# Performance work log

Hardware: AMD Instinct MI355X
Metric: run time of the kernel (lower is better)

Reference implementation:

```python
import jax, jax.numpy as jnp
import numpy as np

LN_EPS = 1e-5

def _ln(x, w, b):
    mu = jnp.mean(x, axis=-1, keepdims=True)
    var = jnp.var(x, axis=-1, keepdims=True)
    return (x - mu) * jax.lax.rsqrt(var + LN_EPS) * w + b

def setup_inputs() -> dict:
    key = jax.random.key(0)
    ks = jax.random.split(key, 16)
    B, T, N = 32, 1024, 77
    D, TD, TE = 512, 256, 2048
    s = lambda fan: 1.0 / np.sqrt(fan)
    return {
        "x": jax.random.normal(ks[0], (B, T, D), jnp.float32),
        "xf": jax.random.normal(ks[1], (B, N, TD), jnp.float32),
        "emb": jax.random.normal(ks[2], (B, TE), jnp.float32),
        "src_mask": jnp.ones((B, T), jnp.float32),
        "cond_type": jax.random.randint(ks[3], (B,), 0, 100, jnp.int64),
        "norm_w": jnp.ones((D,), jnp.float32),
        "norm_b": jnp.zeros((D,), jnp.float32),
        "tnorm_w": jnp.ones((TD,), jnp.float32),
        "tnorm_b": jnp.zeros((TD,), jnp.float32),
        "Wq": jax.random.normal(ks[4], (D, D), jnp.float32) * s(D),
        "bq": jnp.zeros((D,), jnp.float32),
        "Wk": jax.random.normal(ks[5], (D, TD), jnp.float32) * s(TD),
        "bk": jnp.zeros((D,), jnp.float32),
        "Wv": jax.random.normal(ks[6], (D, TD), jnp.float32) * s(TD),
        "bv": jnp.zeros((D,), jnp.float32),
        "emb_w": jax.random.normal(ks[7], (2 * D, TE), jnp.float32) * s(TE),
        "emb_b": jnp.zeros((2 * D,), jnp.float32),
        "snorm_w": jnp.ones((D,), jnp.float32),
        "snorm_b": jnp.zeros((D,), jnp.float32),
        "Wout": jax.random.normal(ks[8], (D, D), jnp.float32) * s(D),
        "bout": jnp.zeros((D,), jnp.float32),
    }

def reference(x, xf, emb, src_mask, cond_type,
              norm_w, norm_b, tnorm_w, tnorm_b,
              Wq, bq, Wk, bk, Wv, bv,
              emb_w, emb_b, snorm_w, snorm_b, Wout, bout):
    B, T, D = x.shape
    N = xf.shape[1]
    H = 8
    dh = D // H
    # projections (no 1/sqrt(dh) scaling, per original)
    q = (_ln(x, norm_w, norm_b) @ Wq.T + bq).reshape(B, T, H, dh)
    xf_n = _ln(xf, tnorm_w, tnorm_b)
    k = (xf_n @ Wk.T + bk).reshape(B, N, H, dh)
    # cond_type gating: text_cond_type = (cond_type % 10 > 0)
    tc = (cond_type % 10 > 0).astype(x.dtype)  # [B]
    bias = (1.0 - tc)[:, None, None, None] * -1000000.0  # [B,1,1,1]
    attn = jnp.einsum('bthd,bnhd->btnh', q, k) + bias
    attn = jax.nn.softmax(attn, axis=2)  # over keys N
    v = (xf_n @ Wv.T + bv) * tc[:, None, None]
    v = v.reshape(B, N, H, dh)
    y = jnp.einsum('btnh,bnhd->bthd', attn, v).reshape(B, T, D)
    # StylizationBlock: silu->linear on emb -> scale/shift, ln, silu->linear, residual
    e = jax.nn.silu(emb) @ emb_w.T + emb_b  # [B, 2D]
    scale, shift = jnp.split(e[:, None, :], 2, axis=2)  # [B,1,D] each
    h = _ln(y, snorm_w, snorm_b) * (1.0 + scale) + shift
    h = jax.nn.silu(h) @ Wout.T + bout
    return x + h
```

## Files before the change

kernel.cpp:

```cpp
#include <hip/hip_runtime.h>
#include <math.h>

#define B_   32
#define T_   1024
#define N_   77
#define D_   512
#define TD_  256
#define TE_  2048
#define H_   8
#define DH_  64

typedef short bf16x8 __attribute__((ext_vector_type(8)));
typedef float f32x4  __attribute__((ext_vector_type(4)));

__device__ __forceinline__ float sigmoidf_fast(float x) {
    return 1.0f / (1.0f + __expf(-x));
}

__device__ __forceinline__ unsigned short f2b(float f) {
    unsigned int u = __float_as_uint(f);
    unsigned int r = u + 0x7FFFu + ((u >> 16) & 1u);
    return (unsigned short)(r >> 16);
}

__device__ __forceinline__ float b2f(short us) {
    return __uint_as_float(((unsigned int)(unsigned short)us) << 16);
}

#define GL16(g, l) __builtin_amdgcn_global_load_lds(                         \
    (const __attribute__((address_space(1))) unsigned int*)(g),              \
    (__attribute__((address_space(3))) unsigned int*)(l), 16, 0, 0)

__global__ __launch_bounds__(256) void ln_xf_kernel(
    const float* __restrict__ x, const float* __restrict__ w, const float* __restrict__ b,
    unsigned short* __restrict__ outb)
{
    int row = blockIdx.x * 4 + (threadIdx.x >> 6);
    int lane = threadIdx.x & 63;
    const float* rp = x + (size_t)row * TD_ + lane * 4;
    float4 v = *(const float4*)rp;
    float s  = v.x + v.y + v.z + v.w;
    float ss = v.x*v.x + v.y*v.y + v.z*v.z + v.w*v.w;
    #pragma unroll
    for (int off = 32; off; off >>= 1) {
        s  += __shfl_xor(s, off);
        ss += __shfl_xor(ss, off);
    }
    float m = s * (1.f / TD_);
    float r = rsqrtf(ss * (1.f / TD_) - m * m + 1e-5f);
    float4 wv = *(const float4*)(w + lane * 4);
    float4 bv = *(const float4*)(b + lane * 4);
    ushort4 o;
    o.x = f2b((v.x - m) * r * wv.x + bv.x);
    o.y = f2b((v.y - m) * r * wv.y + bv.y);
    o.z = f2b((v.z - m) * r * wv.z + bv.z);
    o.w = f2b((v.w - m) * r * wv.w + bv.w);
    *(ushort4*)(outb + (size_t)row * TD_ + lane * 4) = o;
}

__global__ __launch_bounds__(256) void conv_weights_kernel(
    const float* __restrict__ Wq, const float* __restrict__ Wout,
    const float* __restrict__ Wk, const float* __restrict__ Wv,
    unsigned short* __restrict__ wqb, unsigned short* __restrict__ wob,
    unsigned short* __restrict__ wkvb)
{
    int bid = blockIdx.x;
    const float* src; unsigned short* dst;
    if (bid < 128)      { src = Wq;   dst = wqb; }
    else if (bid < 256) { src = Wout; dst = wob;               bid -= 128; }
    else if (bid < 320) { src = Wk;   dst = wkvb;              bid -= 256; }
    else                { src = Wv;   dst = wkvb + D_ * TD_;   bid -= 320; }
    int idx = (bid * 256 + threadIdx.x) * 8;
    float4 v0 = *(const float4*)(src + idx);
    float4 v1 = *(const float4*)(src + idx + 4);
    ushort4 o0 = {f2b(v0.x), f2b(v0.y), f2b(v0.z), f2b(v0.w)};
    ushort4 o1 = {f2b(v1.x), f2b(v1.y), f2b(v1.z), f2b(v1.w)};
    *(ushort4*)(dst + idx)     = o0;
    *(ushort4*)(dst + idx + 4) = o1;
}

__global__ __launch_bounds__(256) void kv_gemm_kernel(
    const unsigned short* __restrict__ Ab,
    const unsigned short* __restrict__ Wb,
    const float* __restrict__ bkp, const float* __restrict__ bvp,
    const int*   __restrict__ cond,
    unsigned short* __restrict__ kout, unsigned short* __restrict__ vout)
{
    constexpr int K = TD_;
    __shared__ __align__(16) unsigned short As[128 * 32];
    __shared__ __align__(16) unsigned short Bs[128 * 32];

    const int tid  = threadIdx.x;
    int id = blockIdx.x;
    int swz = (id & 7) * 20 + (id >> 3);
    const int m0 = (swz >> 3) * 128;
    const int n0 = (swz & 7) * 128;
    const int lane = tid & 63;
    const int w    = tid >> 6;
    const int l15  = lane & 15;
    const int quad = lane >> 4;
    const int wm   = (w >> 1) * 64;
    const int wn   = (w & 1) * 64;

    const int row_a = tid >> 2;
    const int ck    = (tid & 3) ^ ((row_a >> 1) & 3);
    const int sc    = (quad ^ ((l15 >> 1) & 3)) << 3;

    f32x4 acc[4][4];
    #pragma unroll
    for (int i = 0; i < 4; i++)
        #pragma unroll
        for (int j = 0; j < 4; j++)
            acc[i][j] = (f32x4){0.f, 0.f, 0.f, 0.f};

    const char* gAbase = (const char*)Ab + ((size_t)(m0 + row_a) * K) * 2 + ck * 16;
    const char* gBbase = (const char*)Wb + ((size_t)(n0 + row_a) * K) * 2 + ck * 16;
    char* lA = (char*)As + tid * 16;
    char* lB = (char*)Bs + tid * 16;

    for (int k0 = 0; k0 < K; k0 += 32) {
        const char* gA = gAbase + k0 * 2;
        const char* gB = gBbase + k0 * 2;
        GL16(gA, lA);
        GL16(gA + (size_t)64 * K * 2, lA + 4096);
        GL16(gB, lB);
        GL16(gB + (size_t)64 * K * 2, lB + 4096);
        __syncthreads();

        bf16x8 af[4], bfr[4];
        #pragma unroll
        for (int i = 0; i < 4; i++)
            af[i] = *(const bf16x8*)&As[(wm + i * 16 + l15) * 32 + sc];
        #pragma unroll
        for (int j = 0; j < 4; j++)
            bfr[j] = *(const bf16x8*)&Bs[(wn + j * 16 + l15) * 32 + sc];
        #pragma unroll
        for (int i = 0; i < 4; i++)
            #pragma unroll
            for (int j = 0; j < 4; j++)
                acc[i][j] = __builtin_amdgcn_mfma_f32_16x16x32_bf16(af[i], bfr[j], acc[i][j], 0, 0, 0);
        __syncthreads();
    }

    #pragma unroll
    for (int i = 0; i < 4; i++) {
        int mbase = m0 + wm + i * 16 + quad * 4;
        #pragma unroll
        for (int j = 0; j < 4; j++) {
            int n = n0 + wn + j * 16 + l15;
            bool isv = n >= D_;
            int nn = isv ? n - D_ : n;
            float bn = isv ? bvp[nn] : bkp[nn];
            unsigned short* outp = isv ? vout : kout;
            #pragma unroll
            for (int r = 0; r < 4; r++) {
                int m = mbase + r;
                if (m >= B_ * N_) continue;
                float v = acc[i][j][r] + bn;
                if (isv) {
                    int bi = m / N_;
                    v = ((cond[bi] % 10) > 0) ? v : 0.f;
                }
                outp[(size_t)m * D_ + nn] = f2b(v);
            }
        }
    }
}

__global__ __launch_bounds__(256) void emb_gemm_kernel(
    const float* __restrict__ emb, const float* __restrict__ W,
    float* __restrict__ e)
{
    int wid = blockIdx.x * 4 + (threadIdx.x >> 6);
    int lane = threadIdx.x & 63;
    int ngrp = wid >> 3;
    int bgrp = wid & 7;

    float acc[4][4] = {};
    #pragma unroll 2
    for (int it = 0; it < 8; it++) {
        int k = (it * 64 + lane) * 4;
        float4 sv[4], wv[4];
        #pragma unroll
        for (int bi = 0; bi < 4; bi++) {
            float4 t = *(const float4*)&emb[(size_t)(bgrp * 4 + bi) * TE_ + k];
            t.x *= sigmoidf_fast(t.x);
            t.y *= sigmoidf_fast(t.y);
            t.z *= sigmoidf_fast(t.z);
            t.w *= sigmoidf_fast(t.w);
            sv[bi] = t;
        }
        #pragma unroll
        for (int ni = 0; ni < 4; ni++)
            wv[ni] = *(const float4*)&W[(size_t)(ngrp * 4 + ni) * TE_ + k];
        #pragma unroll
        for (int bi = 0; bi < 4; bi++)
            #pragma unroll
            for (int ni = 0; ni < 4; ni++) {
                acc[bi][ni] = fmaf(sv[bi].x, wv[ni].x, acc[bi][ni]);
                acc[bi][ni] = fmaf(sv[bi].y, wv[ni].y, acc[bi][ni]);
                acc[bi][ni] = fmaf(sv[bi].z, wv[ni].z, acc[bi][ni]);
                acc[bi][ni] = fmaf(sv[bi].w, wv[ni].w, acc[bi][ni]);
            }
    }
    #pragma unroll
    for (int bi = 0; bi < 4; bi++)
        #pragma unroll
        for (int ni = 0; ni < 4; ni++) {
            float a = acc[bi][ni];
            #pragma unroll
            for (int off = 32; off; off >>= 1) a += __shfl_xor(a, off);
            if (lane == 0)
                e[(size_t)(bgrp * 4 + bi) * 1024 + ngrp * 4 + ni] = a;
        }
}

__global__ __launch_bounds__(256) void prep_q_kernel(
    const float* __restrict__ x, const float* __restrict__ w, const float* __restrict__ b,
    unsigned short* __restrict__ outb)
{
    int row = blockIdx.x * 4 + (threadIdx.x >> 6);
    int lane = threadIdx.x & 63;
    const float* rp = x + (size_t)row * D_ + lane * 8;
    float4 v0 = *(const float4*)rp;
    float4 v1 = *(const float4*)(rp + 4);
    float s  = v0.x + v0.y + v0.z + v0.w + v1.x + v1.y + v1.z + v1.w;
    float ss = v0.x*v0.x + v0.y*v0.y + v0.z*v0.z + v0.w*v0.w
             + v1.x*v1.x + v1.y*v1.y + v1.z*v1.z + v1.w*v1.w;
    #pragma unroll
    for (int off = 32; off; off >>= 1) {
        s  += __shfl_xor(s, off);
        ss += __shfl_xor(ss, off);
    }
    float m = s * (1.f / D_);
    float r = rsqrtf(ss * (1.f / D_) - m * m + 1e-5f);
    float4 w0 = *(const float4*)(w + lane * 8);
    float4 w1 = *(const float4*)(w + lane * 8 + 4);
    float4 b0 = *(const float4*)(b + lane * 8);
    float4 b1 = *(const float4*)(b + lane * 8 + 4);
    ushort4 o0, o1;
    o0.x = f2b((v0.x - m) * r * w0.x + b0.x);
    o0.y = f2b((v0.y - m) * r * w0.y + b0.y);
    o0.z = f2b((v0.z - m) * r * w0.z + b0.z);
    o0.w = f2b((v0.w - m) * r * w0.w + b0.w);
    o1.x = f2b((v1.x - m) * r * w1.x + b1.x);
    o1.y = f2b((v1.y - m) * r * w1.y + b1.y);
    o1.z = f2b((v1.z - m) * r * w1.z + b1.z);
    o1.w = f2b((v1.w - m) * r * w1.w + b1.w);
    unsigned short* op = outb + (size_t)row * D_ + lane * 8;
    *(ushort4*)op       = o0;
    *(ushort4*)(op + 4) = o1;
}

__global__ __launch_bounds__(256) void prep_h_kernel(
    const unsigned short* __restrict__ y, const float* __restrict__ w, const float* __restrict__ b,
    const float* __restrict__ e, const float* __restrict__ emb_b,
    unsigned short* __restrict__ outb)
{
    int row = blockIdx.x * 4 + (threadIdx.x >> 6);
    int lane = threadIdx.x & 63;
    int bb = row >> 10;
    const unsigned short* rp = y + (size_t)row * D_ + lane * 8;
    bf16x8 yv = *(const bf16x8*)rp;
    float v[8];
    #pragma unroll
    for (int k2 = 0; k2 < 8; k2++) v[k2] = b2f(yv[k2]);
    float s = 0.f, ss = 0.f;
    #pragma unroll
    for (int k2 = 0; k2 < 8; k2++) { s += v[k2]; ss += v[k2] * v[k2]; }
    #pragma unroll
    for (int off = 32; off; off >>= 1) {
        s  += __shfl_xor(s, off);
        ss += __shfl_xor(ss, off);
    }
    float m = s * (1.f / D_);
    float r = rsqrtf(ss * (1.f / D_) - m * m + 1e-5f);
    float4 w0 = *(const float4*)(w + lane * 8);
    float4 w1 = *(const float4*)(w + lane * 8 + 4);
    float4 b0 = *(const float4*)(b + lane * 8);
    float4 b1 = *(const float4*)(b + lane * 8 + 4);
    float wa[8] = {w0.x, w0.y, w0.z, w0.w, w1.x, w1.y, w1.z, w1.w};
    float ba[8] = {b0.x, b0.y, b0.z, b0.w, b1.x, b1.y, b1.z, b1.w};
    const float* ep = e + (size_t)bb * 1024 + lane * 8;
    float4 sc0 = *(const float4*)ep;
    float4 sc1 = *(const float4*)(ep + 4);
    float4 sh0 = *(const float4*)(ep + 512);
    float4 sh1 = *(const float4*)(ep + 512 + 4);
    float4 eb0 = *(const float4*)(emb_b + lane * 8);
    float4 eb1 = *(const float4*)(emb_b + lane * 8 + 4);
    float4 fb0 = *(const float4*)(emb_b + 512 + lane * 8);
    float4 fb1 = *(const float4*)(emb_b + 512 + lane * 8 + 4);
    float sca[8] = {sc0.x + eb0.x, sc0.y + eb0.y, sc0.z + eb0.z, sc0.w + eb0.w,
                    sc1.x + eb1.x, sc1.y + eb1.y, sc1.z + eb1.z, sc1.w + eb1.w};
    float sha[8] = {sh0.x + fb0.x, sh0.y + fb0.y, sh0.z + fb0.z, sh0.w + fb0.w,
                    sh1.x + fb1.x, sh1.y + fb1.y, sh1.z + fb1.z, sh1.w + fb1.w};
    ushort4 o0, o1;
    unsigned short oa[8];
    #pragma unroll
    for (int k2 = 0; k2 < 8; k2++) {
        float hv = ((v[k2] - m) * r * wa[k2] + ba[k2]) * (1.f + sca[k2]) + sha[k2];
        oa[k2] = f2b(hv * sigmoidf_fast(hv));
    }
    o0.x = oa[0]; o0.y = oa[1]; o0.z = oa[2]; o0.w = oa[3];
    o1.x = oa[4]; o1.y = oa[5]; o1.z = oa[6]; o1.w = oa[7];
    unsigned short* op = outb + (size_t)row * D_ + lane * 8;
    *(ushort4*)op       = o0;
    *(ushort4*)(op + 4) = o1;
}

template <int RESID, int OUTBF>
__global__ __launch_bounds__(256) void gemm_bf16_kernel(
    const unsigned short* __restrict__ Ab,
    const unsigned short* __restrict__ Wb,
    const float* __restrict__ bias,
    const float* __restrict__ resid,
    void* __restrict__ Cv)
{
    constexpr int K = 512;
    __shared__ __align__(16) unsigned short As[2][128 * 32];
    __shared__ __align__(16) unsigned short Bs[2][128 * 32];

    const int tid  = threadIdx.x;
    int id = blockIdx.x;
    int swz = (id & 7) * 128 + (id >> 3);
    const int m0 = (swz >> 2) * 128;
    const int n0 = (swz & 3) * 128;
    const int lane = tid & 63;
    const int w    = tid >> 6;
    const int l15  = lane & 15;
    const int quad = lane >> 4;
    const int wm   = (w >> 1) * 64;
    const int wn   = (w & 1) * 64;

    const int row_s = tid >> 2;
    const int ck    = (tid & 3) ^ ((row_s >> 1) & 3);
    const int sc    = (quad ^ ((l15 >> 1) & 3)) << 3;

    f32x4 acc[4][4];
    #pragma unroll
    for (int i = 0; i < 4; i++)
        #pragma unroll
        for (int j = 0; j < 4; j++)
            acc[i][j] = (f32x4){0.f, 0.f, 0.f, 0.f};

    const char* gA = (const char*)Ab + ((size_t)(m0 + row_s) * K) * 2 + ck * 16;
    const char* gB = (const char*)Wb + ((size_t)(n0 + row_s) * K) * 2 + ck * 16;
    const size_t g2 = (size_t)64 * K * 2;
    char* lA = (char*)&As[0][0] + tid * 16;
    char* lB = (char*)&Bs[0][0] + tid * 16;

#define STAGE_G(s, buf) do {                                                  \
        GL16(gA + (s) * 64,      lA + (buf) * 8192);                          \
        GL16(gA + (s) * 64 + g2, lA + (buf) * 8192 + 4096);                   \
        GL16(gB + (s) * 64,      lB + (buf) * 8192);                          \
        GL16(gB + (s) * 64 + g2, lB + (buf) * 8192 + 4096);                   \
    } while (0)

    bf16x8 af[4], bfr[4];
#define LOADF_G(buf) do {                                                     \
        _Pragma("unroll")                                                     \
        for (int i = 0; i < 4; i++)                                           \
            af[i] = *(const bf16x8*)&As[buf][(wm + i * 16 + l15) * 32 + sc];  \
        _Pragma("unroll")                                                     \
        for (int j = 0; j < 4; j++)                                           \
            bfr[j] = *(const bf16x8*)&Bs[buf][(wn + j * 16 + l15) * 32 + sc]; \
    } while (0)

#define MFMA_G() do {                                                         \
        _Pragma("unroll")                                                     \
        for (int i = 0; i < 4; i++)                                           \
            _Pragma("unroll")                                                 \
            for (int j = 0; j < 4; j++)                                       \
                acc[i][j] = __builtin_amdgcn_mfma_f32_16x16x32_bf16(af[i], bfr[j], acc[i][j], 0, 0, 0); \
    } while (0)

    STAGE_G(0, 0);
    __syncthreads();

    #pragma unroll 1
    for (int t = 0; t < 8; t++) {
        LOADF_G(0);
        STAGE_G(2 * t + 1, 1);
        MFMA_G();
        __syncthreads();
        LOADF_G(1);
        if (t < 7) STAGE_G(2 * t + 2, 0);
        MFMA_G();
        __syncthreads();
    }
#undef STAGE_G
#undef LOADF_G
#undef MFMA_G

    float* C = (float*)Cv;
    unsigned short* Cb = (unsigned short*)Cv;
    #pragma unroll
    for (int i = 0; i < 4; i++) {
        int mbase = m0 + wm + i * 16 + quad * 4;
        #pragma unroll
        for (int j = 0; j < 4; j++) {
            int n = n0 + wn + j * 16 + l15;
            float bn = bias[n];
            #pragma unroll
            for (int r = 0; r < 4; r++) {
                size_t off = (size_t)(mbase + r) * 512 + n;
                float v = acc[i][j][r] + bn;
                if (RESID) v += resid[off];
                if (OUTBF) Cb[off] = f2b(v);
                else       C[off]  = v;
            }
        }
    }
}

#define KS2   0
#define VT2   5760
#define PS2   11904
#define SMEM2 18560

__global__ __launch_bounds__(256) void attn_mfma2_kernel(
    const unsigned short* __restrict__ qb,
    const unsigned short* __restrict__ kb,
    const unsigned short* __restrict__ vb,
    unsigned short* __restrict__ yout)
{
    __shared__ __align__(16) unsigned short smem[SMEM2];

    const int tid = threadIdx.x;
    const int t0 = blockIdx.x * 64;
    const int h  = blockIdx.y;
    const int b  = blockIdx.z;

    const int lane = tid & 63;
    const int w    = tid >> 6;
    const int l15  = lane & 15;
    const int quad = lane >> 4;
    const int koff = quad * 8;
    const int mrow = w * 16 + l15;

    const unsigned short* qrow = qb + ((size_t)(b * T_ + t0 + mrow)) * D_ + h * 64 + koff;
    bf16x8 aq0 = *(const bf16x8*)qrow;
    bf16x8 aq1 = *(const bf16x8*)(qrow + 32);

    const unsigned short* kbase = kb + ((size_t)(b * N_)) * D_ + h * 64;
    #pragma unroll
    for (int i = 0; i < 3; i++) {
        int idx = tid + i * 256;
        if (idx < 640) {
            int row = idx >> 3, c8 = idx & 7;
            bf16x8 v = (bf16x8){0, 0, 0, 0, 0, 0, 0, 0};
            if (row < N_) v = *(const bf16x8*)(kbase + (size_t)row * D_ + c8 * 8);
            *(bf16x8*)&smem[KS2 + row * 72 + c8 * 8] = v;
        }
    }
    const unsigned short* vbase = vb + ((size_t)(b * N_)) * D_ + h * 64;
    #pragma unroll
    for (int i = 0; i < 3; i++) {
        int idx = tid + i * 256;
        if (idx < 616) {
            int n = idx >> 3, c8 = idx & 7;
            bf16x8 v = *(const bf16x8*)(vbase + (size_t)n * D_ + c8 * 8);
            int cn = n >> 3, wn = n & 7;
            #pragma unroll
            for (int j = 0; j < 8; j++) {
                int d = c8 * 8 + j;
                int s2 = (j ^ c8) & 3;
                smem[VT2 + d * 96 + ((cn ^ s2) << 3) + wn] = v[j];
            }
        }
    }
    if (tid < 128) {
        int d = tid >> 1, c = 10 + (tid & 1);
        int s2 = (d ^ (d >> 3)) & 3;
        *(bf16x8*)&smem[VT2 + d * 96 + ((c ^ s2) << 3)] = (bf16x8){0, 0, 0, 0, 0, 0, 0, 0};
    }
    {
        int d = tid >> 2, t = tid & 3;
        if (t < 3) {
            int s2 = (d ^ (d >> 3)) & 3;
            smem[VT2 + d * 96 + ((9 ^ s2) << 3) + 5 + t] = 0;
        }
    }
    #pragma unroll
    for (int i = 0; i < 4; i++) {
        int idx = tid + i * 256;
        int row = idx >> 4, col = 80 + (idx & 15);
        smem[PS2 + row * 104 + col] = 0;
    }
    __syncthreads();

    float s[5][4];
    #pragma unroll
    for (int nt = 0; nt < 5; nt++) {
        bf16x8 bk0 = *(const bf16x8*)&smem[KS2 + (nt * 16 + l15) * 72 + koff];
        bf16x8 bk1 = *(const bf16x8*)&smem[KS2 + (nt * 16 + l15) * 72 + 32 + koff];
        f32x4 c = {0.f, 0.f, 0.f, 0.f};
        c = __builtin_amdgcn_mfma_f32_16x16x32_bf16(aq0, bk0, c, 0, 0, 0);
        c = __builtin_amdgcn_mfma_f32_16x16x32_bf16(aq1, bk1, c, 0, 0, 0);
        #pragma unroll
        for (int r = 0; r < 4; r++) s[nt][r] = c[r];
    }
    if (l15 >= N_ - 64) {
        #pragma unroll
        for (int r = 0; r < 4; r++) s[4][r] = -1e30f;
    }
    float li[4];
    #pragma unroll
    for (int r = 0; r < 4; r++) {
        float m = s[0][r];
        #pragma unroll
        for (int nt = 1; nt < 5; nt++) m = fmaxf(m, s[nt][r]);
        m = fmaxf(m, __shfl_xor(m, 1));
        m = fmaxf(m, __shfl_xor(m, 2));
        m = fmaxf(m, __shfl_xor(m, 4));
        m = fmaxf(m, __shfl_xor(m, 8));
        float l = 0.f;
        #pragma unroll
        for (int nt = 0; nt < 5; nt++) {
            float ev = __expf(s[nt][r] - m);
            s[nt][r] = ev;
            l += ev;
        }
        l += __shfl_xor(l, 1);
        l += __shfl_xor(l, 2);
        l += __shfl_xor(l, 4);
        l += __shfl_xor(l, 8);
        li[r] = 1.f / l;
    }
    #pragma unroll
    for (int r = 0; r < 4; r++) {
        int prow = w * 16 + quad * 4 + r;
        #pragma unroll
        for (int nt = 0; nt < 5; nt++) {
            smem[PS2 + prow * 104 + nt * 16 + l15] = f2b(s[nt][r] * li[r]);
        }
    }

    bf16x8 pa0 = *(const bf16x8*)&smem[PS2 + mrow * 104 + 0  + koff];
    bf16x8 pa1 = *(const bf16x8*)&smem[PS2 + mrow * 104 + 32 + koff];
    bf16x8 pa2 = *(const bf16x8*)&smem[PS2 + mrow * 104 + 64 + koff];

    unsigned short* obase = yout + ((size_t)(b * T_ + t0 + w * 16)) * D_ + h * 64;
    #pragma unroll
    for (int dt = 0; dt < 4; dt++) {
        int drow = dt * 16 + l15;
        int s2 = (drow ^ (drow >> 3)) & 3;
        bf16x8 bv0 = *(const bf16x8*)&smem[VT2 + drow * 96 + (((0 + quad) ^ s2) << 3)];
        bf16x8 bv1 = *(const bf16x8*)&smem[VT2 + drow * 96 + (((4 + quad) ^ s2) << 3)];
        bf16x8 bv2 = *(const bf16x8*)&smem[VT2 + drow * 96 + (((8 + quad) ^ s2) << 3)];
        f32x4 c = {0.f, 0.f, 0.f, 0.f};
        c = __builtin_amdgcn_mfma_f32_16x16x32_bf16(pa0, bv0, c, 0, 0, 0);
        c = __builtin_amdgcn_mfma_f32_16x16x32_bf16(pa1, bv1, c, 0, 0, 0);
        c = __builtin_amdgcn_mfma_f32_16x16x32_bf16(pa2, bv2, c, 0, 0, 0);
        #pragma unroll
        for (int r = 0; r < 4; r++) {
            obase[(size_t)(quad * 4 + r) * D_ + dt * 16 + l15] = f2b(c[r]);
        }
    }
}

extern "C" void kernel_launch(void* const* d_in, const int* in_sizes, int n_in,
                              void* d_out, int out_size, void* d_ws, size_t ws_size,
                              hipStream_t stream)
{
    const float* x       = (const float*)d_in[0];
    const float* xf      = (const float*)d_in[1];
    const float* emb     = (const float*)d_in[2];
    const int*   cond    = (const int*)d_in[4];
    const float* norm_w  = (const float*)d_in[5];
    const float* norm_b  = (const float*)d_in[6];
    const float* tnorm_w = (const float*)d_in[7];
    const float* tnorm_b = (const float*)d_in[8];
    const float* Wq      = (const float*)d_in[9];
    const float* bq      = (const float*)d_in[10];
    const float* Wk      = (const float*)d_in[11];
    const float* bk      = (const float*)d_in[12];
    const float* Wv      = (const float*)d_in[13];
    const float* bv      = (const float*)d_in[14];
    const float* emb_w   = (const float*)d_in[15];
    const float* emb_b   = (const float*)d_in[16];
    const float* snorm_w = (const float*)d_in[17];
    const float* snorm_b = (const float*)d_in[18];
    const float* Wout    = (const float*)d_in[19];
    const float* bout    = (const float*)d_in[20];
    float* out = (float*)d_out;

    float* ws = (float*)d_ws;
    float* ebuf = ws;
    unsigned short* u = (unsigned short*)(ebuf + (size_t)B_ * 2 * D_);
    unsigned short* qyb  = u;  u += (size_t)B_ * T_ * D_;
    unsigned short* xfnb = u;  u += (size_t)2560 * TD_;
    unsigned short* kb16 = u;  u += (size_t)B_ * N_ * D_;
    unsigned short* vb16 = u;  u += (size_t)B_ * N_ * D_;
    unsigned short* abh  = u;  u += (size_t)B_ * T_ * D_;
    unsigned short* wqb  = u;  u += (size_t)D_ * D_;
    unsigned short* wob  = u;  u += (size_t)D_ * D_;
    unsigned short* wkvb = u;  u += (size_t)2 * D_ * TD_;
    unsigned short* qb = (unsigned short*)d_out;

    const int BT = B_ * T_;
    const int BN = B_ * N_;

    ln_xf_kernel<<<BN / 4, 256, 0, stream>>>(xf, tnorm_w, tnorm_b, xfnb);
    conv_weights_kernel<<<384, 256, 0, stream>>>(Wq, Wout, Wk, Wv, wqb, wob, wkvb);
    kv_gemm_kernel<<<160, 256, 0, stream>>>(xfnb, wkvb, bk, bv, cond, kb16, vb16);
    prep_q_kernel<<<BT / 4, 256, 0, stream>>>(x, norm_w, norm_b, abh);
    gemm_bf16_kernel<0, 1><<<1024, 256, 0, stream>>>(abh, wqb, bq, nullptr, qb);
    emb_gemm_kernel<<<512, 256, 0, stream>>>(emb, emb_w, ebuf);
    {
        dim3 grid(T_ / 64, H_, B_);
        attn_mfma2_kernel<<<grid, 256, 0, stream>>>(qb, kb16, vb16, qyb);
    }
    prep_h_kernel<<<BT / 4, 256, 0, stream>>>(qyb, snorm_w, snorm_b, ebuf, emb_b, abh);
    gemm_bf16_kernel<1, 0><<<1024, 256, 0, stream>>>(abh, wob, bout, x, out);
}
```

Baseline: 308.4 us.

## Use triple-buffered LDS pipeline with explicit vmcnt waits in GEMM kernels

Both the KV projection GEMM and the main bf16 GEMM now stage three K-slices ahead into a three-deep LDS ring. Each step waits only on the oldest load group via s_waitcnt vmcnt instead of a full __syncthreads drain. Sched barriers pin the ordering, and loops are fully unrolled. This aims to hide global-load latency behind MFMA work, at the cost of 50% more LDS per block, which may reduce occupancy.

```diff
diff --git a/kernel.cpp b/kernel.cpp
--- a/kernel.cpp
+++ b/kernel.cpp
@@ -30,6 +30,13 @@
 #define GL16(g, l) __builtin_amdgcn_global_load_lds(                         \
     (const __attribute__((address_space(1))) unsigned int*)(g),              \
     (__attribute__((address_space(3))) unsigned int*)(l), 16, 0, 0)
+
+#define WAITV8() asm volatile("s_waitcnt vmcnt(8)" ::: "memory")
+#define WAITV4() asm volatile("s_waitcnt vmcnt(4)" ::: "memory")
+#define WAITV0() asm volatile("s_waitcnt vmcnt(0)" ::: "memory")
+#define WAITL0() asm volatile("s_waitcnt lgkmcnt(0)" ::: "memory")
+#define SBAR()   __builtin_amdgcn_s_barrier()
+#define SCHED0() __builtin_amdgcn_sched_barrier(0)
 
 __global__ __launch_bounds__(256) void ln_xf_kernel(
     const float* __restrict__ x, const float* __restrict__ w, const float* __restrict__ b,
@@ -87,8 +94,9 @@
     unsigned short* __restrict__ kout, unsigned short* __restrict__ vout)
 {
     constexpr int K = TD_;
-    __shared__ __align__(16) unsigned short As[128 * 32];
-    __shared__ __align__(16) unsigned short Bs[128 * 32];
+    constexpr int NSTEP = 8;
+    __shared__ __align__(16) unsigned short As[3][128 * 32];
+    __shared__ __align__(16) unsigned short Bs[3][128 * 32];
 
     const int tid  = threadIdx.x;
     int id = blockIdx.x;
@@ -113,34 +121,47 @@
         for (int j = 0; j < 4; j++)
             acc[i][j] = (f32x4){0.f, 0.f, 0.f, 0.f};
 
-    const char* gAbase = (const char*)Ab + ((size_t)(m0 + row_a) * K) * 2 + ck * 16;
-    const char* gBbase = (const char*)Wb + ((size_t)(n0 + row_a) * K) * 2 + ck * 16;
-    char* lA = (char*)As + tid * 16;
-    char* lB = (char*)Bs + tid * 16;
-
-    for (int k0 = 0; k0 < K; k0 += 32) {
-        const char* gA = gAbase + k0 * 2;
-        const char* gB = gBbase + k0 * 2;
-        GL16(gA, lA);
-        GL16(gA + (size_t)64 * K * 2, lA + 4096);
-        GL16(gB, lB);
-        GL16(gB + (size_t)64 * K * 2, lB + 4096);
-        __syncthreads();
-
-        bf16x8 af[4], bfr[4];
+    const char* gA = (const char*)Ab + ((size_t)(m0 + row_a) * K) * 2 + ck * 16;
+    const char* gB = (const char*)Wb + ((size_t)(n0 + row_a) * K) * 2 + ck * 16;
+    const size_t g2 = (size_t)64 * K * 2;
+    char* lA = (char*)&As[0][0] + tid * 16;
+    char* lB = (char*)&Bs[0][0] + tid * 16;
+
+#define KSTAGE(s, buf) do {                                                   \
+        GL16(gA + (s) * 64,      lA + (buf) * 8192);                          \
+        GL16(gA + (s) * 64 + g2, lA + (buf) * 8192 + 4096);                   \
+        GL16(gB + (s) * 64,      lB + (buf) * 8192);                          \
+        GL16(gB + (s) * 64 + g2, lB + (buf) * 8192 + 4096);                   \
+    } while (0)
+
+    KSTAGE(0, 0);
+    KSTAGE(1, 1);
+    KSTAGE(2, 2);
+
+    bf16x8 af[4], bfr[4];
+    #pragma unroll
+    for (int t = 0; t < NSTEP; t++) {
+        const int cur = t % 3;
+        if (t < NSTEP - 2)       { WAITV8(); }
+        else if (t == NSTEP - 2) { WAITV4(); }
+        else                     { WAITV0(); }
+        SBAR(); SCHED0();
         #pragma unroll
         for (int i = 0; i < 4; i++)
-            af[i] = *(const bf16x8*)&As[(wm + i * 16 + l15) * 32 + sc];
+            af[i] = *(const bf16x8*)&As[cur][(wm + i * 16 + l15) * 32 + sc];
         #pragma unroll
         for (int j = 0; j < 4; j++)
-            bfr[j] = *(const bf16x8*)&Bs[(wn + j * 16 + l15) * 32 + sc];
+            bfr[j] = *(const bf16x8*)&Bs[cur][(wn + j * 16 + l15) * 32 + sc];
+        WAITL0(); SCHED0();
+        SBAR(); SCHED0();
+        if (t + 3 < NSTEP) KSTAGE(t + 3, cur);
         #pragma unroll
         for (int i = 0; i < 4; i++)
             #pragma unroll
             for (int j = 0; j < 4; j++)
                 acc[i][j] = __builtin_amdgcn_mfma_f32_16x16x32_bf16(af[i], bfr[j], acc[i][j], 0, 0, 0);
-        __syncthreads();
-    }
+    }
+#undef KSTAGE
 
     #pragma unroll
     for (int i = 0; i < 4; i++) {
@@ -317,8 +338,9 @@
     void* __restrict__ Cv)
 {
     constexpr int K = 512;
-    __shared__ __align__(16) unsigned short As[2][128 * 32];
-    __shared__ __align__(16) unsigned short Bs[2][128 * 32];
+    constexpr int NSTEP = 16;
+    __shared__ __align__(16) unsigned short As[3][128 * 32];
+    __shared__ __align__(16) unsigned short Bs[3][128 * 32];
 
     const int tid  = threadIdx.x;
     int id = blockIdx.x;
@@ -356,41 +378,34 @@
         GL16(gB + (s) * 64 + g2, lB + (buf) * 8192 + 4096);                   \
     } while (0)
 
+    STAGE_G(0, 0);
+    STAGE_G(1, 1);
+    STAGE_G(2, 2);
+
     bf16x8 af[4], bfr[4];
-#define LOADF_G(buf) do {                                                     \
-        _Pragma("unroll")                                                     \
-        for (int i = 0; i < 4; i++)                                           \
-            af[i] = *(const bf16x8*)&As[buf][(wm + i * 16 + l15) * 32 + sc];  \
-        _Pragma("unroll")                                                     \
-        for (int j = 0; j < 4; j++)                                           \
-            bfr[j] = *(const bf16x8*)&Bs[buf][(wn + j * 16 + l15) * 32 + sc]; \
-    } while (0)
-
-#define MFMA_G() do {                                                         \
-        _Pragma("unroll")                                                     \
-        for (int i = 0; i < 4; i++)                                           \
-            _Pragma("unroll")                                                 \
-            for (int j = 0; j < 4; j++)                                       \
-                acc[i][j] = __builtin_amdgcn_mfma_f32_16x16x32_bf16(af[i], bfr[j], acc[i][j], 0, 0, 0); \
-    } while (0)
-
-    STAGE_G(0, 0);
-    __syncthreads();
-
-    #pragma unroll 1
-    for (int t = 0; t < 8; t++) {
-        LOADF_G(0);
-        STAGE_G(2 * t + 1, 1);
-        MFMA_G();
-        __syncthreads();
-        LOADF_G(1);
-        if (t < 7) STAGE_G(2 * t + 2, 0);
-        MFMA_G();
-        __syncthreads();
+    #pragma unroll
+    for (int t = 0; t < NSTEP; t++) {
+        const int cur = t % 3;
+        if (t < NSTEP - 2)       { WAITV8(); }
+        else if (t == NSTEP - 2) { WAITV4(); }
+        else                     { WAITV0(); }
+        SBAR(); SCHED0();
+        #pragma unroll
+        for (int i = 0; i < 4; i++)
+            af[i] = *(const bf16x8*)&As[cur][(wm + i * 16 + l15) * 32 + sc];
+        #pragma unroll
+        for (int j = 0; j < 4; j++)
+            bfr[j] = *(const bf16x8*)&Bs[cur][(wn + j * 16 + l15) * 32 + sc];
+        WAITL0(); SCHED0();
+        SBAR(); SCHED0();
+        if (t + 3 < NSTEP) STAGE_G(t + 3, cur);
+        #pragma unroll
+        for (int i = 0; i < 4; i++)
+            #pragma unroll
+            for (int j = 0; j < 4; j++)
+                acc[i][j] = __builtin_amdgcn_mfma_f32_16x16x32_bf16(af[i], bfr[j], acc[i][j], 0, 0, 0);
     }
 #undef STAGE_G
-#undef LOADF_G
-#undef MFMA_G
 
     float* C = (float*)Cv;
     unsigned short* Cb = (unsigned short*)Cv;
```

After: 299.9 us. 2.7% less time.
